# Performance work log

Measured on AMD Instinct MI355X. Metric: run time of the kernel, lower is better.

Reference implementation:

```python
import jax, jax.numpy as jnp
import numpy as np

B, N, K = 4096, 200, 64
H1, H2 = 80, 40
NEG = -4294967295.0  # -2**32 + 1, as in the original


def prelu(x, alpha):
    return jnp.where(x > 0, x, alpha * x)


def setup_inputs() -> dict:
    key = jax.random.key(0)
    ks = jax.random.split(key, 12)
    query = jax.random.normal(ks[0], (B, K), dtype=jnp.float32)
    seq_key = jax.random.normal(ks[1], (B, N, K), dtype=jnp.float32)
    value = jax.random.normal(ks[2], (B, N, K), dtype=jnp.float32)
    mask = jax.random.randint(ks[3], (B, N), 0, 2, dtype=jnp.int32)
    din = 4 * K  # concat of [q, k, q-k, q*k]
    W1 = jax.random.normal(ks[4], (din, H1), dtype=jnp.float32) / np.sqrt(din)
    b1 = jnp.zeros((H1,), dtype=jnp.float32)
    a1 = jnp.full((H1,), 0.25, dtype=jnp.float32)  # PReLU alpha
    W2 = jax.random.normal(ks[5], (H1, H2), dtype=jnp.float32) / np.sqrt(H1)
    b2 = jnp.zeros((H2,), dtype=jnp.float32)
    a2 = jnp.full((H2,), 0.25, dtype=jnp.float32)
    Wo = jax.random.normal(ks[6], (H2, 1), dtype=jnp.float32) / np.sqrt(H2)
    bo = jnp.zeros((1,), dtype=jnp.float32)
    return {"query": query, "key": seq_key, "value": value, "mask": mask,
            "W1": W1, "b1": b1, "a1": a1, "W2": W2, "b2": b2, "a2": a2,
            "Wo": Wo, "bo": bo}


def reference(query, key, value, mask, W1, b1, a1, W2, b2, a2, Wo, bo):
    # query: [B, K] -> tiled to [B, N, K]
    q = jnp.broadcast_to(query[:, None, :], key.shape)
    # DIN feature: [B, N, 4K]
    emb = jnp.concatenate([q, key, q - key, q * key], axis=-1)
    h = prelu(jnp.einsum('bnd,dh->bnh', emb, W1) + b1, a1)   # [B, N, H1]
    h = prelu(jnp.einsum('bnd,dh->bnh', h, W2) + b2, a2)     # [B, N, H2]
    score = (jnp.einsum('bnd,do->bno', h, Wo) + bo)[..., 0]   # [B, N]
    score = jnp.where(mask == 0, NEG, score)
    score = jax.nn.softmax(score, axis=-1)
    out = jnp.einsum('bn,bnk->bk', score, value)              # [B, K]
    return out
```

## Files before the change

kernel.cpp:

```cpp
#include <hip/hip_runtime.h>
#include <math.h>

#define B_SZ 4096
#define N_SZ 200
#define K_SZ 64
#define H1 80
#define H2 40
#define NEG_V (-4294967295.0f)

#define NW1FRAG 10
#define NW2FRAG 9
#define W1ELT (NW1FRAG * 512)
#define W2HALVES (NW2FRAG * 512)
#define WLDS_HALVES (W1ELT + W2HALVES)

typedef _Float16 f16x8 __attribute__((ext_vector_type(8)));
typedef float f32x4 __attribute__((ext_vector_type(4)));
typedef unsigned int u32;

union H2U { _Float16 h[2]; u32 u; };
union U4F { u32 u[4]; f16x8 v; };

typedef __attribute__((address_space(3))) u32 lds_u32;
typedef const __attribute__((address_space(1))) u32 glb_u32;

__device__ __forceinline__ void gload16(const void* gp, void* lp) {
    __builtin_amdgcn_global_load_lds((glb_u32*)gp, (lds_u32*)lp, 16, 0, 0);
}

__global__ __launch_bounds__(128) void qw_kernel(const float* __restrict__ query,
                                                 const float* __restrict__ W1,
                                                 const float* __restrict__ b1,
                                                 float* __restrict__ qW) {
    int b = blockIdx.x;
    int tid = threadIdx.x;
    __shared__ float sq[K_SZ];
    if (tid < K_SZ) sq[tid] = query[b * K_SZ + tid];
    __syncthreads();
    if (tid < H1) {
        float acc = b1[tid];
#pragma unroll 8
        for (int i = 0; i < K_SZ; ++i)
            acc += sq[i] * (W1[i * H1 + tid] + W1[(128 + i) * H1 + tid]);
        qW[b * H1 + tid] = acc;
    }
}

__global__ __launch_bounds__(256) void prep_bp(const float* __restrict__ W1,
                                               const float* __restrict__ W2,
                                               float* __restrict__ W1kG,
                                               float* __restrict__ W1pG,
                                               _Float16* __restrict__ Bp2) {
    int idx = blockIdx.x * 256 + threadIdx.x;
    if (idx < W1ELT) {
        int j = idx & 7, lane = (idx >> 3) & 63, f = idx >> 9;
        int ks = f & 1, ht = f >> 1;
        int k = ks * 32 + (lane >> 4) * 8 + j;
        int h = ht * 16 + (lane & 15);
        W1kG[idx] = W1[(64 + k) * H1 + h] - W1[(128 + k) * H1 + h];
        W1pG[idx] = W1[(192 + k) * H1 + h];
    } else {
        int idx2 = idx - W1ELT;
        if (idx2 < W2HALVES) {
            int j = idx2 & 7, lane = (idx2 >> 3) & 63, f2 = idx2 >> 9;
            int ks2 = f2 % 3, ht2 = f2 / 3;
            int k2 = ks2 * 32 + (lane >> 4) * 8 + j;
            int m = ht2 * 16 + (lane & 15);
            float w = (k2 < H1 && m < H2) ? W2[k2 * H2 + m] : 0.0f;
            Bp2[idx2] = (_Float16)w;
        }
    }
}

__global__ __launch_bounds__(256, 4) void fused_kernel(
    const float* __restrict__ query, const float* __restrict__ key,
    const float* __restrict__ value, const int* __restrict__ mask,
    const float* __restrict__ W1kG, const float* __restrict__ W1pG,
    const _Float16* __restrict__ Bp2G,
    const float* __restrict__ a1, const float* __restrict__ b2,
    const float* __restrict__ a2, const float* __restrict__ Wo,
    const float* __restrict__ bo, const float* __restrict__ qW,
    float* __restrict__ out) {
    __shared__ _Float16 wlds[WLDS_HALVES];
    __shared__ float sq[K_SZ];
    __shared__ float sqW[H1];
    __shared__ float sa1[H1];
    __shared__ float sb2[48], sa2[48], sWo[48];
    __shared__ float sprob[256];
    __shared__ float sred[8];
    __shared__ float spart[4 * K_SZ];

    const int tid = threadIdx.x;
    const int wv = tid >> 6;
    const int l = tid & 63;
    const int l15 = l & 15;
    const int lg = l >> 4;
    const int b = blockIdx.x;
    const int p0 = b * N_SZ;
    const int NT = (wv == 0) ? 4 : 3;
    const int tb = (wv == 0) ? 0 : 1 + wv * 3;

    {
#pragma unroll
        for (int i = 0; i < 2; ++i) {
            int cb = i * 256 + wv * 64;
            gload16(&Bp2G[(size_t)(cb + l) * 8], (char*)&wlds[W1ELT] + (size_t)cb * 16);
        }
        if (wv == 0) {
            int cb = 512;
            gload16(&Bp2G[(size_t)(cb + l) * 8], (char*)&wlds[W1ELT] + (size_t)cb * 16);
        }
    }

    if (tid < K_SZ) sq[tid] = query[b * K_SZ + tid];
    if (tid < H1) { sqW[tid] = qW[b * H1 + tid]; sa1[tid] = a1[tid]; }
    if (tid >= 128 && tid < 176) {
        int i = tid - 128;
        sb2[i] = (i < H2) ? b2[i] : 0.0f;
        sa2[i] = (i < H2) ? a2[i] : 0.0f;
        sWo[i] = (i < H2) ? Wo[i] : 0.0f;
    }
    float bov = bo[0];
    __syncthreads();

#pragma unroll
    for (int r = 0; r < 20; ++r) {
        int idx = r * 256 + tid;
        int j = idx & 7, lane = (idx >> 3) & 63, f = idx >> 9;
        int k = (f & 1) * 32 + ((lane >> 4) * 8) + j;
        float w = W1kG[idx] + sq[k] * W1pG[idx];
        wlds[idx] = (_Float16)w;
    }
    __syncthreads();

    const int wofs = l * 8;

    f16x8 Bk[4][2];
#pragma unroll
    for (int i = 0; i < 4; ++i) {
        if (i < NT) {
            int nloc = (tb + i) * 16 + l15;
            int pg = p0 + nloc;
            int pgc = (pg < B_SZ * N_SZ) ? pg : (B_SZ * N_SZ - 1);
#pragma unroll
            for (int ksp = 0; ksp < 2; ++ksp) {
                const float* kp = &key[(size_t)pgc * K_SZ + ksp * 32 + lg * 8];
                float4 k0 = *reinterpret_cast<const float4*>(kp);
                float4 k1 = *reinterpret_cast<const float4*>(kp + 4);
                f16x8 bk;
                bk[0] = (_Float16)k0.x; bk[1] = (_Float16)k0.y; bk[2] = (_Float16)k0.z; bk[3] = (_Float16)k0.w;
                bk[4] = (_Float16)k1.x; bk[5] = (_Float16)k1.y; bk[6] = (_Float16)k1.z; bk[7] = (_Float16)k1.w;
                Bk[i][ksp] = bk;
            }
        }
    }

    f32x4 D1[4][5];
#pragma unroll
    for (int i = 0; i < 4; ++i)
#pragma unroll
        for (int ht = 0; ht < 5; ++ht) D1[i][ht] = (f32x4){0.f, 0.f, 0.f, 0.f};
#pragma unroll
    for (int ht = 0; ht < 5; ++ht) {
#pragma unroll
        for (int ks = 0; ks < 2; ++ks) {
            f16x8 wh = *reinterpret_cast<const f16x8*>(&wlds[(ht * 2 + ks) * 512 + wofs]);
#pragma unroll
            for (int i = 0; i < 4; ++i) {
                if (i < NT) {
                    D1[i][ht] = __builtin_amdgcn_mfma_f32_16x16x32_f16(wh, Bk[i][ks], D1[i][ht], 0, 0, 0);
                }
            }
        }
    }

    u32 pk[4][6][2];
#pragma unroll
    for (int i = 0; i < 4; ++i) {
        if (i < NT) {
#pragma unroll
            for (int ht = 0; ht < 5; ++ht) {
                float4 qw4 = *reinterpret_cast<const float4*>(&sqW[ht * 16 + lg * 4]);
                float4 aa4 = *reinterpret_cast<const float4*>(&sa1[ht * 16 + lg * 4]);
                float h0 = D1[i][ht][0] + qw4.x;
                float h1v = D1[i][ht][1] + qw4.y;
                float h2 = D1[i][ht][2] + qw4.z;
                float h3 = D1[i][ht][3] + qw4.w;
                h0 = (h0 > 0.f) ? h0 : h0 * aa4.x;
                h1v = (h1v > 0.f) ? h1v : h1v * aa4.y;
                h2 = (h2 > 0.f) ? h2 : h2 * aa4.z;
                h3 = (h3 > 0.f) ? h3 : h3 * aa4.w;
                H2U u0, u1;
                u0.h[0] = (_Float16)h0; u0.h[1] = (_Float16)h1v;
                u1.h[0] = (_Float16)h2; u1.h[1] = (_Float16)h3;
                pk[i][ht][0] = u0.u;
                pk[i][ht][1] = u1.u;
            }
            pk[i][5][0] = 0u; pk[i][5][1] = 0u;
        }
    }

    f32x4 D2[4][3];
#pragma unroll
    for (int i = 0; i < 4; ++i)
#pragma unroll
        for (int ht = 0; ht < 3; ++ht) D2[i][ht] = (f32x4){0.f, 0.f, 0.f, 0.f};
#pragma unroll
    for (int ks2 = 0; ks2 < 3; ++ks2) {
        f16x8 B2f[4];
#pragma unroll
        for (int i = 0; i < 4; ++i) {
            if (i < NT) {
                U4F bu;
#pragma unroll
                for (int q = 0; q < 4; ++q) {
                    int src = ((lg * 2 + (q >> 1)) & 3) * 16 + l15;
                    u32 va = (u32)__shfl((int)pk[i][ks2 * 2][q & 1], src, 64);
                    u32 vb = (u32)__shfl((int)pk[i][ks2 * 2 + 1][q & 1], src, 64);
                    bu.u[q] = (lg < 2) ? va : vb;
                }
                B2f[i] = bu.v;
            }
        }
#pragma unroll
        for (int ht2 = 0; ht2 < 3; ++ht2) {
            f16x8 wh = *reinterpret_cast<const f16x8*>(&wlds[W1ELT + (ht2 * 3 + ks2) * 512 + wofs]);
#pragma unroll
            for (int i = 0; i < 4; ++i) {
                if (i < NT) {
                    D2[i][ht2] = __builtin_amdgcn_mfma_f32_16x16x32_f16(wh, B2f[i], D2[i][ht2], 0, 0, 0);
                }
            }
        }
    }

#pragma unroll
    for (int i = 0; i < 4; ++i) {
        if (i < NT) {
            float psum = 0.f;
#pragma unroll
            for (int ht2 = 0; ht2 < 3; ++ht2) {
                float4 b4 = *reinterpret_cast<const float4*>(&sb2[ht2 * 16 + lg * 4]);
                float4 a4 = *reinterpret_cast<const float4*>(&sa2[ht2 * 16 + lg * 4]);
                float4 w4 = *reinterpret_cast<const float4*>(&sWo[ht2 * 16 + lg * 4]);
                float v0 = D2[i][ht2][0] + b4.x;
                float v1 = D2[i][ht2][1] + b4.y;
                float v2 = D2[i][ht2][2] + b4.z;
                float v3 = D2[i][ht2][3] + b4.w;
                v0 = (v0 > 0.f) ? v0 : v0 * a4.x;
                v1 = (v1 > 0.f) ? v1 : v1 * a4.y;
                v2 = (v2 > 0.f) ? v2 : v2 * a4.z;
                v3 = (v3 > 0.f) ? v3 : v3 * a4.w;
                psum += v0 * w4.x + v1 * w4.y + v2 * w4.z + v3 * w4.w;
            }
            psum += __shfl_xor(psum, 16);
            psum += __shfl_xor(psum, 32);
            if (lg == 0) {
                int nloc = (tb + i) * 16 + l15;
                float sv;
                if (nloc < N_SZ) sv = (mask[p0 + nloc] == 0) ? NEG_V : (psum + bov);
                else sv = -INFINITY;
                sprob[nloc] = sv;
            }
        }
    }
    __syncthreads();

    float s = (tid < 208) ? sprob[tid] : -INFINITY;
    float m = s;
#pragma unroll
    for (int off = 32; off >= 1; off >>= 1) m = fmaxf(m, __shfl_xor(m, off));
    if ((tid & 63) == 0) sred[tid >> 6] = m;
    __syncthreads();
    m = fmaxf(fmaxf(sred[0], sred[1]), fmaxf(sred[2], sred[3]));

    float e = (tid < 208) ? expf(s - m) : 0.0f;
    sprob[tid] = e;
    float t = e;
#pragma unroll
    for (int off = 32; off >= 1; off >>= 1) t += __shfl_xor(t, off);
    if ((tid & 63) == 0) sred[4 + (tid >> 6)] = t;
    __syncthreads();
    float inv = 1.0f / (sred[4] + sred[5] + sred[6] + sred[7]);

    {
        const int n0 = wv * 50;
        const int g = lg;
        const int kc = l15 * 4;
        float4 vr[13];
#pragma unroll
        for (int q = 0; q < 13; ++q) {
            int sub = q * 4 + g;
            int row = n0 + ((sub < 50) ? sub : 49);
            vr[q] = *reinterpret_cast<const float4*>(
                &value[((size_t)p0 + row) * K_SZ + kc]);
        }
        f32x4 vacc = (f32x4){0.f, 0.f, 0.f, 0.f};
#pragma unroll
        for (int q = 0; q < 13; ++q) {
            int sub = q * 4 + g;
            float w = (sub < 50) ? sprob[n0 + sub] : 0.0f;
            vacc[0] += w * vr[q].x;
            vacc[1] += w * vr[q].y;
            vacc[2] += w * vr[q].z;
            vacc[3] += w * vr[q].w;
        }
#pragma unroll
        for (int e = 0; e < 4; ++e) {
            vacc[e] += __shfl_xor(vacc[e], 16);
            vacc[e] += __shfl_xor(vacc[e], 32);
        }
        if (lg == 0) {
            float4 vout = {vacc[0], vacc[1], vacc[2], vacc[3]};
            *reinterpret_cast<float4*>(&spart[wv * K_SZ + kc]) = vout;
        }
    }
    __syncthreads();
    if (tid < K_SZ) {
        out[b * K_SZ + tid] =
            (spart[tid] + spart[64 + tid] + spart[128 + tid] + spart[192 + tid]) * inv;
    }
}

extern "C" void kernel_launch(void* const* d_in, const int* in_sizes, int n_in,
                              void* d_out, int out_size, void* d_ws, size_t ws_size,
                              hipStream_t stream) {
    const float* query = (const float*)d_in[0];
    const float* key   = (const float*)d_in[1];
    const float* value = (const float*)d_in[2];
    const int*   mask  = (const int*)d_in[3];
    const float* W1    = (const float*)d_in[4];
    const float* b1    = (const float*)d_in[5];
    const float* a1    = (const float*)d_in[6];
    const float* W2    = (const float*)d_in[7];
    const float* b2    = (const float*)d_in[8];
    const float* a2    = (const float*)d_in[9];
    const float* Wo    = (const float*)d_in[10];
    const float* bo    = (const float*)d_in[11];
    float* out = (float*)d_out;

    float* qW      = (float*)d_ws;
    float* W1kG    = qW + (size_t)B_SZ * H1;
    float* W1pG    = W1kG + W1ELT;
    _Float16* Bp2  = (_Float16*)(W1pG + W1ELT);

    qw_kernel<<<B_SZ, 128, 0, stream>>>(query, W1, b1, qW);
    prep_bp<<<(W1ELT + W2HALVES + 255) / 256, 256, 0, stream>>>(W1, W2, W1kG, W1pG, Bp2);
    fused_kernel<<<B_SZ, 256, 0, stream>>>(
        query, key, value, mask, W1kG, W1pG, Bp2, a1, b2, a2, Wo, bo, qW, out);
}
```

Baseline: 130.8 us.

## Process four batches per block with double-buffered key prefetch

Each block now loops over four batch rows instead of one, which amortises the W2 LDS fill and constant setup across rows. The next batch's keys are loaded into a second register buffer while the current batch runs its layer-2 MFMA and softmax work. Launch bounds drop occupancy to 3 blocks per SM, since the doubled key registers raise register pressure. The grid is cut to 1024 blocks, which gives fewer blocks for latency hiding across CUs and adds an extra barrier per iteration.

```diff
diff --git a/kernel.cpp b/kernel.cpp
--- a/kernel.cpp
+++ b/kernel.cpp
@@ -8,11 +8,10 @@
 #define H2 40
 #define NEG_V (-4294967295.0f)
 
-#define NW1FRAG 10
-#define NW2FRAG 9
-#define W1ELT (NW1FRAG * 512)
-#define W2HALVES (NW2FRAG * 512)
+#define W1ELT 5120
+#define W2HALVES 4608
 #define WLDS_HALVES (W1ELT + W2HALVES)
+#define BPB 4
 
 typedef _Float16 f16x8 __attribute__((ext_vector_type(8)));
 typedef float f32x4 __attribute__((ext_vector_type(4)));
@@ -72,7 +71,31 @@
     }
 }
 
-__global__ __launch_bounds__(256, 4) void fused_kernel(
+__device__ __forceinline__ void load_keys(const float* __restrict__ key,
+                                          const float* __restrict__ ,
+                                          int p0, int tb, int NT, int l15, int lg,
+                                          f16x8 Bk[4][2]) {
+#pragma unroll
+    for (int i = 0; i < 4; ++i) {
+        if (i < NT) {
+            int nloc = (tb + i) * 16 + l15;
+            int pg = p0 + nloc;
+            int pgc = (pg < B_SZ * N_SZ) ? pg : (B_SZ * N_SZ - 1);
+#pragma unroll
+            for (int ksp = 0; ksp < 2; ++ksp) {
+                const float* kp = &key[(size_t)pgc * K_SZ + ksp * 32 + lg * 8];
+                float4 k0 = *reinterpret_cast<const float4*>(kp);
+                float4 k1 = *reinterpret_cast<const float4*>(kp + 4);
+                f16x8 bk;
+                bk[0] = (_Float16)k0.x; bk[1] = (_Float16)k0.y; bk[2] = (_Float16)k0.z; bk[3] = (_Float16)k0.w;
+                bk[4] = (_Float16)k1.x; bk[5] = (_Float16)k1.y; bk[6] = (_Float16)k1.z; bk[7] = (_Float16)k1.w;
+                Bk[i][ksp] = bk;
+            }
+        }
+    }
+}
+
+__global__ __launch_bounds__(256, 3) void fused_kernel(
     const float* __restrict__ query, const float* __restrict__ key,
     const float* __restrict__ value, const int* __restrict__ mask,
     const float* __restrict__ W1kG, const float* __restrict__ W1pG,
@@ -95,8 +118,7 @@
     const int l = tid & 63;
     const int l15 = l & 15;
     const int lg = l >> 4;
-    const int b = blockIdx.x;
-    const int p0 = b * N_SZ;
+    const int bb0 = blockIdx.x * BPB;
     const int NT = (wv == 0) ? 4 : 3;
     const int tb = (wv == 0) ? 0 : 1 + wv * 3;
 
@@ -111,9 +133,7 @@
             gload16(&Bp2G[(size_t)(cb + l) * 8], (char*)&wlds[W1ELT] + (size_t)cb * 16);
         }
     }
-
-    if (tid < K_SZ) sq[tid] = query[b * K_SZ + tid];
-    if (tid < H1) { sqW[tid] = qW[b * H1 + tid]; sa1[tid] = a1[tid]; }
+    if (tid < H1) sa1[tid] = a1[tid];
     if (tid >= 128 && tid < 176) {
         int i = tid - 128;
         sb2[i] = (i < H2) ? b2[i] : 0.0f;
@@ -121,204 +141,201 @@
         sWo[i] = (i < H2) ? Wo[i] : 0.0f;
     }
     float bov = bo[0];
-    __syncthreads();
-
-#pragma unroll
-    for (int r = 0; r < 20; ++r) {
-        int idx = r * 256 + tid;
-        int j = idx & 7, lane = (idx >> 3) & 63, f = idx >> 9;
-        int k = (f & 1) * 32 + ((lane >> 4) * 8) + j;
-        float w = W1kG[idx] + sq[k] * W1pG[idx];
-        wlds[idx] = (_Float16)w;
-    }
-    __syncthreads();
 
     const int wofs = l * 8;
 
-    f16x8 Bk[4][2];
-#pragma unroll
-    for (int i = 0; i < 4; ++i) {
-        if (i < NT) {
-            int nloc = (tb + i) * 16 + l15;
-            int pg = p0 + nloc;
-            int pgc = (pg < B_SZ * N_SZ) ? pg : (B_SZ * N_SZ - 1);
-#pragma unroll
-            for (int ksp = 0; ksp < 2; ++ksp) {
-                const float* kp = &key[(size_t)pgc * K_SZ + ksp * 32 + lg * 8];
-                float4 k0 = *reinterpret_cast<const float4*>(kp);
-                float4 k1 = *reinterpret_cast<const float4*>(kp + 4);
-                f16x8 bk;
-                bk[0] = (_Float16)k0.x; bk[1] = (_Float16)k0.y; bk[2] = (_Float16)k0.z; bk[3] = (_Float16)k0.w;
-                bk[4] = (_Float16)k1.x; bk[5] = (_Float16)k1.y; bk[6] = (_Float16)k1.z; bk[7] = (_Float16)k1.w;
-                Bk[i][ksp] = bk;
-            }
-        }
-    }
-
-    f32x4 D1[4][5];
-#pragma unroll
-    for (int i = 0; i < 4; ++i)
-#pragma unroll
-        for (int ht = 0; ht < 5; ++ht) D1[i][ht] = (f32x4){0.f, 0.f, 0.f, 0.f};
-#pragma unroll
-    for (int ht = 0; ht < 5; ++ht) {
-#pragma unroll
-        for (int ks = 0; ks < 2; ++ks) {
-            f16x8 wh = *reinterpret_cast<const f16x8*>(&wlds[(ht * 2 + ks) * 512 + wofs]);
+    f16x8 Bkb[2][4][2];
+    load_keys(key, nullptr, bb0 * N_SZ, tb, NT, l15, lg, Bkb[0]);
+
+#pragma unroll
+    for (int it = 0; it < BPB; ++it) {
+        const int b = bb0 + it;
+        const int p0 = b * N_SZ;
+
+        if (tid < K_SZ) sq[tid] = query[(size_t)b * K_SZ + tid];
+        if (tid < H1) sqW[tid] = qW[(size_t)b * H1 + tid];
+        __syncthreads();
+
+#pragma unroll
+        for (int r = 0; r < 20; ++r) {
+            int idx = r * 256 + tid;
+            int j = idx & 7, lane = (idx >> 3) & 63, f = idx >> 9;
+            int k = (f & 1) * 32 + ((lane >> 4) * 8) + j;
+            float w = W1kG[idx] + sq[k] * W1pG[idx];
+            wlds[idx] = (_Float16)w;
+        }
+        __syncthreads();
+
+        f32x4 D1[4][5];
+#pragma unroll
+        for (int i = 0; i < 4; ++i)
+#pragma unroll
+            for (int ht = 0; ht < 5; ++ht) D1[i][ht] = (f32x4){0.f, 0.f, 0.f, 0.f};
+#pragma unroll
+        for (int ht = 0; ht < 5; ++ht) {
+#pragma unroll
+            for (int ks = 0; ks < 2; ++ks) {
+                f16x8 wh = *reinterpret_cast<const f16x8*>(&wlds[(ht * 2 + ks) * 512 + wofs]);
+#pragma unroll
+                for (int i = 0; i < 4; ++i) {
+                    if (i < NT) {
+                        D1[i][ht] = __builtin_amdgcn_mfma_f32_16x16x32_f16(
+                            wh, Bkb[it & 1][i][ks], D1[i][ht], 0, 0, 0);
+                    }
+                }
+            }
+        }
+
+        if (it < BPB - 1) {
+            load_keys(key, nullptr, (b + 1) * N_SZ, tb, NT, l15, lg, Bkb[(it + 1) & 1]);
+        }
+
+        u32 pk[4][6][2];
+#pragma unroll
+        for (int i = 0; i < 4; ++i) {
+            if (i < NT) {
+#pragma unroll
+                for (int ht = 0; ht < 5; ++ht) {
+                    float4 qw4 = *reinterpret_cast<const float4*>(&sqW[ht * 16 + lg * 4]);
+                    float4 aa4 = *reinterpret_cast<const float4*>(&sa1[ht * 16 + lg * 4]);
+                    float h0 = D1[i][ht][0] + qw4.x;
+                    float h1v = D1[i][ht][1] + qw4.y;
+                    float h2 = D1[i][ht][2] + qw4.z;
+                    float h3 = D1[i][ht][3] + qw4.w;
+                    h0 = (h0 > 0.f) ? h0 : h0 * aa4.x;
+                    h1v = (h1v > 0.f) ? h1v : h1v * aa4.y;
+                    h2 = (h2 > 0.f) ? h2 : h2 * aa4.z;
+                    h3 = (h3 > 0.f) ? h3 : h3 * aa4.w;
+                    H2U u0, u1;
+                    u0.h[0] = (_Float16)h0; u0.h[1] = (_Float16)h1v;
+                    u1.h[0] = (_Float16)h2; u1.h[1] = (_Float16)h3;
+                    pk[i][ht][0] = u0.u;
+                    pk[i][ht][1] = u1.u;
+                }
+                pk[i][5][0] = 0u; pk[i][5][1] = 0u;
+            }
+        }
+
+        f32x4 D2[4][3];
+#pragma unroll
+        for (int i = 0; i < 4; ++i)
+#pragma unroll
+            for (int ht = 0; ht < 3; ++ht) D2[i][ht] = (f32x4){0.f, 0.f, 0.f, 0.f};
+#pragma unroll
+        for (int ks2 = 0; ks2 < 3; ++ks2) {
+            f16x8 B2f[4];
 #pragma unroll
             for (int i = 0; i < 4; ++i) {
                 if (i < NT) {
-                    D1[i][ht] = __builtin_amdgcn_mfma_f32_16x16x32_f16(wh, Bk[i][ks], D1[i][ht], 0, 0, 0);
-                }
-            }
-        }
-    }
-
-    u32 pk[4][6][2];
-#pragma unroll
-    for (int i = 0; i < 4; ++i) {
-        if (i < NT) {
-#pragma unroll
-            for (int ht = 0; ht < 5; ++ht) {
-                float4 qw4 = *reinterpret_cast<const float4*>(&sqW[ht * 16 + lg * 4]);
-                float4 aa4 = *reinterpret_cast<const float4*>(&sa1[ht * 16 + lg * 4]);
-                float h0 = D1[i][ht][0] + qw4.x;
-                float h1v = D1[i][ht][1] + qw4.y;
-                float h2 = D1[i][ht][2] + qw4.z;
-                float h3 = D1[i][ht][3] + qw4.w;
-                h0 = (h0 > 0.f) ? h0 : h0 * aa4.x;
-                h1v = (h1v > 0.f) ? h1v : h1v * aa4.y;
-                h2 = (h2 > 0.f) ? h2 : h2 * aa4.z;
-                h3 = (h3 > 0.f) ? h3 : h3 * aa4.w;
-                H2U u0, u1;
-                u0.h[0] = (_Float16)h0; u0.h[1] = (_Float16)h1v;
-                u1.h[0] = (_Float16)h2; u1.h[1] = (_Float16)h3;
-                pk[i][ht][0] = u0.u;
-                pk[i][ht][1] = u1.u;
-            }
-            pk[i][5][0] = 0u; pk[i][5][1] = 0u;
-        }
-    }
-
-    f32x4 D2[4][3];
-#pragma unroll
-    for (int i = 0; i < 4; ++i)
-#pragma unroll
-        for (int ht = 0; ht < 3; ++ht) D2[i][ht] = (f32x4){0.f, 0.f, 0.f, 0.f};
-#pragma unroll
-    for (int ks2 = 0; ks2 < 3; ++ks2) {
-        f16x8 B2f[4];
+                    U4F bu;
+#pragma unroll
+                    for (int q = 0; q < 4; ++q) {
+                        int src = ((lg * 2 + (q >> 1)) & 3) * 16 + l15;
+                        u32 va = (u32)__shfl((int)pk[i][ks2 * 2][q & 1], src, 64);
+                        u32 vb = (u32)__shfl((int)pk[i][ks2 * 2 + 1][q & 1], src, 64);
+                        bu.u[q] = (lg < 2) ? va : vb;
+                    }
+                    B2f[i] = bu.v;
+                }
+            }
+#pragma unroll
+            for (int ht2 = 0; ht2 < 3; ++ht2) {
+                f16x8 wh = *reinterpret_cast<const f16x8*>(&wlds[W1ELT + (ht2 * 3 + ks2) * 512 + wofs]);
+#pragma unroll
+                for (int i = 0; i < 4; ++i) {
+                    if (i < NT) {
+                        D2[i][ht2] = __builtin_amdgcn_mfma_f32_16x16x32_f16(wh, B2f[i], D2[i][ht2], 0, 0, 0);
+                    }
+                }
+            }
+        }
+
 #pragma unroll
         for (int i = 0; i < 4; ++i) {
             if (i < NT) {
-                U4F bu;
-#pragma unroll
-                for (int q = 0; q < 4; ++q) {
-                    int src = ((lg * 2 + (q >> 1)) & 3) * 16 + l15;
-                    u32 va = (u32)__shfl((int)pk[i][ks2 * 2][q & 1], src, 64);
-                    u32 vb = (u32)__shfl((int)pk[i][ks2 * 2 + 1][q & 1], src, 64);
-                    bu.u[q] = (lg < 2) ? va : vb;
-                }
-                B2f[i] = bu.v;
-            }
-        }
-#pragma unroll
-        for (int ht2 = 0; ht2 < 3; ++ht2) {
-            f16x8 wh = *reinterpret_cast<const f16x8*>(&wlds[W1ELT + (ht2 * 3 + ks2) * 512 + wofs]);
-#pragma unroll
-            for (int i = 0; i < 4; ++i) {
-                if (i < NT) {
-                    D2[i][ht2] = __builtin_amdgcn_mfma_f32_16x16x32_f16(wh, B2f[i], D2[i][ht2], 0, 0, 0);
-                }
-            }
-        }
-    }
-
-#pragma unroll
-    for (int i = 0; i < 4; ++i) {
-        if (i < NT) {
-            float psum = 0.f;
-#pragma unroll
-            for (int ht2 = 0; ht2 < 3; ++ht2) {
-                float4 b4 = *reinterpret_cast<const float4*>(&sb2[ht2 * 16 + lg * 4]);
-                float4 a4 = *reinterpret_cast<const float4*>(&sa2[ht2 * 16 + lg * 4]);
-                float4 w4 = *reinterpret_cast<const float4*>(&sWo[ht2 * 16 + lg * 4]);
-                float v0 = D2[i][ht2][0] + b4.x;
-                float v1 = D2[i][ht2][1] + b4.y;
-                float v2 = D2[i][ht2][2] + b4.z;
-                float v3 = D2[i][ht2][3] + b4.w;
-                v0 = (v0 > 0.f) ? v0 : v0 * a4.x;
-                v1 = (v1 > 0.f) ? v1 : v1 * a4.y;
-                v2 = (v2 > 0.f) ? v2 : v2 * a4.z;
-                v3 = (v3 > 0.f) ? v3 : v3 * a4.w;
-                psum += v0 * w4.x + v1 * w4.y + v2 * w4.z + v3 * w4.w;
-            }
-            psum += __shfl_xor(psum, 16);
-            psum += __shfl_xor(psum, 32);
+                float psum = 0.f;
+#pragma unroll
+                for (int ht2 = 0; ht2 < 3; ++ht2) {
+                    float4 b4 = *reinterpret_cast<const float4*>(&sb2[ht2 * 16 + lg * 4]);
+                    float4 a4 = *reinterpret_cast<const float4*>(&sa2[ht2 * 16 + lg * 4]);
+                    float4 w4 = *reinterpret_cast<const float4*>(&sWo[ht2 * 16 + lg * 4]);
+                    float v0 = D2[i][ht2][0] + b4.x;
+                    float v1 = D2[i][ht2][1] + b4.y;
+                    float v2 = D2[i][ht2][2] + b4.z;
+                    float v3 = D2[i][ht2][3] + b4.w;
+                    v0 = (v0 > 0.f) ? v0 : v0 * a4.x;
+                    v1 = (v1 > 0.f) ? v1 : v1 * a4.y;
+                    v2 = (v2 > 0.f) ? v2 : v2 * a4.z;
+                    v3 = (v3 > 0.f) ? v3 : v3 * a4.w;
+                    psum += v0 * w4.x + v1 * w4.y + v2 * w4.z + v3 * w4.w;
+                }
+                psum += __shfl_xor(psum, 16);
+                psum += __shfl_xor(psum, 32);
+                if (lg == 0) {
+                    int nloc = (tb + i) * 16 + l15;
+                    float sv;
+                    if (nloc < N_SZ) sv = (mask[p0 + nloc] == 0) ? NEG_V : (psum + bov);
+                    else sv = -INFINITY;
+                    sprob[nloc] = sv;
+                }
+            }
+        }
+        __syncthreads();
+
+        float s = (tid < 208) ? sprob[tid] : -INFINITY;
+        float m = s;
+#pragma unroll
+        for (int off = 32; off >= 1; off >>= 1) m = fmaxf(m, __shfl_xor(m, off));
+        if ((tid & 63) == 0) sred[tid >> 6] = m;
+        __syncthreads();
+        m = fmaxf(fmaxf(sred[0], sred[1]), fmaxf(sred[2], sred[3]));
+
+        float e = (tid < 208) ? expf(s - m) : 0.0f;
+        sprob[tid] = e;
+        float t = e;
+#pragma unroll
+        for (int off = 32; off >= 1; off >>= 1) t += __shfl_xor(t, off);
+        if ((tid & 63) == 0) sred[4 + (tid >> 6)] = t;
+        __syncthreads();
+        float inv = 1.0f / (sred[4] + sred[5] + sred[6] + sred[7]);
+
+        {
+            const int n0 = wv * 50;
+            const int kc = l15 * 4;
+            float4 vr[13];
+#pragma unroll
+            for (int q = 0; q < 13; ++q) {
+                int sub = q * 4 + lg;
+                int row = n0 + ((sub < 50) ? sub : 49);
+                vr[q] = *reinterpret_cast<const float4*>(
+                    &value[((size_t)p0 + row) * K_SZ + kc]);
+            }
+            f32x4 vacc = (f32x4){0.f, 0.f, 0.f, 0.f};
+#pragma unroll
+            for (int q = 0; q < 13; ++q) {
+                int sub = q * 4 + lg;
+                float w = (sub < 50) ? sprob[n0 + sub] : 0.0f;
+                vacc[0] += w * vr[q].x;
+                vacc[1] += w * vr[q].y;
+                vacc[2] += w * vr[q].z;
+                vacc[3] += w * vr[q].w;
+            }
+#pragma unroll
+            for (int e2 = 0; e2 < 4; ++e2) {
+                vacc[e2] += __shfl_xor(vacc[e2], 16);
+                vacc[e2] += __shfl_xor(vacc[e2], 32);
+            }
             if (lg == 0) {
-                int nloc = (tb + i) * 16 + l15;
-                float sv;
-                if (nloc < N_SZ) sv = (mask[p0 + nloc] == 0) ? NEG_V : (psum + bov);
-                else sv = -INFINITY;
-                sprob[nloc] = sv;
-            }
-        }
-    }
-    __syncthreads();
-
-    float s = (tid < 208) ? sprob[tid] : -INFINITY;
-    float m = s;
-#pragma unroll
-    for (int off = 32; off >= 1; off >>= 1) m = fmaxf(m, __shfl_xor(m, off));
-    if ((tid & 63) == 0) sred[tid >> 6] = m;
-    __syncthreads();
-    m = fmaxf(fmaxf(sred[0], sred[1]), fmaxf(sred[2], sred[3]));
-
-    float e = (tid < 208) ? expf(s - m) : 0.0f;
-    sprob[tid] = e;
-    float t = e;
-#pragma unroll
-    for (int off = 32; off >= 1; off >>= 1) t += __shfl_xor(t, off);
-    if ((tid & 63) == 0) sred[4 + (tid >> 6)] = t;
-    __syncthreads();
-    float inv = 1.0f / (sred[4] + sred[5] + sred[6] + sred[7]);
-
-    {
-        const int n0 = wv * 50;
-        const int g = lg;
-        const int kc = l15 * 4;
-        float4 vr[13];
-#pragma unroll
-        for (int q = 0; q < 13; ++q) {
-            int sub = q * 4 + g;
-            int row = n0 + ((sub < 50) ? sub : 49);
-            vr[q] = *reinterpret_cast<const float4*>(
-                &value[((size_t)p0 + row) * K_SZ + kc]);
-        }
-        f32x4 vacc = (f32x4){0.f, 0.f, 0.f, 0.f};
-#pragma unroll
-        for (int q = 0; q < 13; ++q) {
-            int sub = q * 4 + g;
-            float w = (sub < 50) ? sprob[n0 + sub] : 0.0f;
-            vacc[0] += w * vr[q].x;
-            vacc[1] += w * vr[q].y;
-            vacc[2] += w * vr[q].z;
-            vacc[3] += w * vr[q].w;
-        }
-#pragma unroll
-        for (int e = 0; e < 4; ++e) {
-            vacc[e] += __shfl_xor(vacc[e], 16);
-            vacc[e] += __shfl_xor(vacc[e], 32);
-        }
-        if (lg == 0) {
-            float4 vout = {vacc[0], vacc[1], vacc[2], vacc[3]};
-            *reinterpret_cast<float4*>(&spart[wv * K_SZ + kc]) = vout;
-        }
-    }
-    __syncthreads();
-    if (tid < K_SZ) {
-        out[b * K_SZ + tid] =
-            (spart[tid] + spart[64 + tid] + spart[128 + tid] + spart[192 + tid]) * inv;
+                float4 vout = {vacc[0], vacc[1], vacc[2], vacc[3]};
+                *reinterpret_cast<float4*>(&spart[wv * K_SZ + kc]) = vout;
+            }
+        }
+        __syncthreads();
+        if (tid < K_SZ) {
+            out[(size_t)b * K_SZ + tid] =
+                (spart[tid] + spart[64 + tid] + spart[128 + tid] + spart[192 + tid]) * inv;
+        }
+        __syncthreads();
     }
 }
 
@@ -346,6 +363,6 @@
 
     qw_kernel<<<B_SZ, 128, 0, stream>>>(query, W1, b1, qW);
     prep_bp<<<(W1ELT + W2HALVES + 255) / 256, 256, 0, stream>>>(W1, W2, W1kG, W1pG, Bp2);
-    fused_kernel<<<B_SZ, 256, 0, stream>>>(
+    fused_kernel<<<B_SZ / BPB, 256, 0, stream>>>(
         query, key, value, mask, W1kG, W1pG, Bp2, a1, b2, a2, Wo, bo, qW, out);
 }
```

Result: slower. 390.9 us (+198.9%).
